# Kernel optimization log

Measured on AMD Instinct MI355X. Metric: run time of the kernel, lower is better.

Reference implementation:

```python
import jax, jax.numpy as jnp
import numpy as np

D_MODEL = 1024

def setup_inputs() -> dict:
    key = jax.random.key(0)
    k1, k2, k3, k4, k5 = jax.random.split(key, 5)
    x = jax.random.normal(k1, (4, 2048, D_MODEL), dtype=jnp.float32)
    # torch nn.Linear weights: [out_features, in_features]
    W_qkv = jax.random.normal(k2, (3 * D_MODEL, D_MODEL), dtype=jnp.float32) * (1.0 / np.sqrt(D_MODEL))
    b_qkv = jax.random.normal(k3, (3 * D_MODEL,), dtype=jnp.float32) * 0.01
    W_proj = jax.random.normal(k4, (D_MODEL, D_MODEL), dtype=jnp.float32) * (1.0 / np.sqrt(D_MODEL))
    b_proj = jax.random.normal(k5, (D_MODEL,), dtype=jnp.float32) * 0.01
    return {"x": x, "W_qkv": W_qkv, "b_qkv": b_qkv, "W_proj": W_proj, "b_proj": b_proj}

def reference(x, W_qkv, b_qkv, W_proj, b_proj):
    # qkv projection: x @ W.T + b  (torch Linear convention)
    qkv = jnp.einsum('bsd,ed->bse', x, W_qkv) + b_qkv  # [B,S,3D]
    q, k, v = jnp.split(qkv, 3, axis=-1)               # each [B,S,D]
    scale = 1.0 / jnp.sqrt(jnp.asarray(q.shape[-1], dtype=q.dtype))
    scores = jnp.einsum('bqd,bkd->bqk', q, k) * scale   # [B,S,S]
    attn = jax.nn.softmax(scores, axis=-1)
    out = jnp.einsum('bqk,bkd->bqd', attn, v)           # [B,S,D]
    return jnp.einsum('bsd,ed->bse', out, W_proj) + b_proj
```

## Files before the change

### kernel.cpp

```cpp
#include <hip/hip_runtime.h>
#include <stdint.h>
#include <stddef.h>


typedef __attribute__((ext_vector_type(8))) short bf16x8;
typedef __attribute__((ext_vector_type(4))) float f32x4;

__device__ __forceinline__ unsigned short f2bf(float f) {
  unsigned u = __float_as_uint(f);
  u += 0x7fffu + ((u >> 16) & 1u);
  return (unsigned short)(u >> 16);
}
__device__ __forceinline__ float bf2f(unsigned short h) {
  return __uint_as_float(((unsigned)h) << 16);
}

typedef const __attribute__((address_space(1))) void* gas_ptr;
typedef __attribute__((address_space(3))) void* las_ptr;

__device__ __forceinline__ void gload_lds16(const void* g, void* l) {
  __builtin_amdgcn_global_load_lds((gas_ptr)(uintptr_t)g,
                                   (las_ptr)(uint32_t)(uintptr_t)l, 16, 0, 0);
}

__device__ __forceinline__ f32x4 mfma16(bf16x8 a, bf16x8 b, f32x4 c) {
  return __builtin_amdgcn_mfma_f32_16x16x32_bf16(a, b, c, 0, 0, 0);
}

__global__ __launch_bounds__(256) void cvt_f32_bf16(
    const float* __restrict__ in, unsigned short* __restrict__ out, int n) {
  int i = (blockIdx.x * blockDim.x + threadIdx.x) * 4;
  int stride = gridDim.x * blockDim.x * 4;
  for (; i < n; i += stride) {
    float4 v = *reinterpret_cast<const float4*>(in + i);
    ushort4 o;
    o.x = f2bf(v.x); o.y = f2bf(v.y); o.z = f2bf(v.z); o.w = f2bf(v.w);
    *reinterpret_cast<ushort4*>(out + i) = o;
  }
}

__device__ __forceinline__ void stage_gf(const unsigned short* __restrict__ P,
                                         int ld, unsigned short* dst, int wid,
                                         int lane) {
#pragma unroll
  for (int c = 0; c < 4; ++c) {
    int s = (c * 4 + wid) * 64 + lane;
    int row = s >> 3, g = s & 7;
    gload_lds16(P + (size_t)row * ld + ((g ^ (row & 7)) * 8),
                dst + (c * 4 + wid) * 512);
  }
}

template <bool OUT_BF16, bool HAS_BIAS, bool EXPOUT, bool RSCALE,
          bool TRANSOUT, bool RSUM>
__global__ __launch_bounds__(256, 2) void gf(
    const unsigned short* __restrict__ A, const unsigned short* __restrict__ B,
    void* __restrict__ Cv, const float* __restrict__ bias,
    const float* __restrict__ rowsc, float* __restrict__ rsum, int rsStride,
    int K, int lda, int ldb, int ldc,
    long long strideA, long long strideB, long long strideC, float alpha) {
  __shared__ unsigned short lds[2][2][128 * 64];

  const int bz = blockIdx.z;
  const int gx = gridDim.x;
  int lin = blockIdx.y * gx + blockIdx.x;
  int bx, by;
  {
    const int nwg = gx * gridDim.y;
    const int q = nwg >> 3;
    lin = (lin & 7) * q + (lin >> 3);
    const int t = lin >> 6, r = lin & 63;
    const int tilesX = gx >> 3;
    bx = (t % tilesX) * 8 + (r & 7);
    by = (t / tilesX) * 8 + (r >> 3);
  }
  const int rowBase = by * 128;
  const int colBase = bx * 128;

  const unsigned short* Ap = A + (size_t)bz * (size_t)strideA + (size_t)rowBase * lda;
  const unsigned short* Bp = B + (size_t)bz * (size_t)strideB + (size_t)colBase * ldb;

  const int tid = threadIdx.x;
  const int wid = tid >> 6;
  const int lane = tid & 63;
  const int wr = wid >> 1;
  const int wc = wid & 1;
  const int fr = lane & 15;
  const int kgi = lane >> 4;

  const int nt = K >> 6;

  f32x4 acc[4][4] = {};

  stage_gf(Ap, lda, &lds[0][0][0], wid, lane);
  stage_gf(Bp, ldb, &lds[0][1][0], wid, lane);
  asm volatile("s_waitcnt vmcnt(0)" ::: "memory");
  __builtin_amdgcn_sched_barrier(0);
  __builtin_amdgcn_s_barrier();

  for (int t = 0; t < nt; ++t) {
    const int cur = t & 1;
    if (t + 1 < nt) {
      stage_gf(Ap + (size_t)(t + 1) * 64, lda, &lds[cur ^ 1][0][0], wid, lane);
      stage_gf(Bp + (size_t)(t + 1) * 64, ldb, &lds[cur ^ 1][1][0], wid, lane);
    }
    const unsigned short* sAc = &lds[cur][0][0];
    const unsigned short* sBc = &lds[cur][1][0];

    bf16x8 af[4][2], bv[4][2];
#pragma unroll
    for (int m = 0; m < 4; ++m) {
      int row = wr * 64 + m * 16 + fr;
      int r7 = row & 7;
      af[m][0] = *(const bf16x8*)&sAc[row * 64 + ((kgi ^ r7) * 8)];
      af[m][1] = *(const bf16x8*)&sAc[row * 64 + (((4 + kgi) ^ r7) * 8)];
    }
#pragma unroll
    for (int n = 0; n < 4; ++n) {
      int row = wc * 64 + n * 16 + fr;
      int r7 = row & 7;
      bv[n][0] = *(const bf16x8*)&sBc[row * 64 + ((kgi ^ r7) * 8)];
      bv[n][1] = *(const bf16x8*)&sBc[row * 64 + (((4 + kgi) ^ r7) * 8)];
    }
    asm volatile("s_waitcnt lgkmcnt(0)" ::: "memory");
    __builtin_amdgcn_sched_barrier(0);
    __builtin_amdgcn_s_setprio(1);
#pragma unroll
    for (int m = 0; m < 4; ++m)
#pragma unroll
      for (int n = 0; n < 4; ++n) {
        acc[m][n] = mfma16(af[m][0], bv[n][0], acc[m][n]);
        acc[m][n] = mfma16(af[m][1], bv[n][1], acc[m][n]);
      }
    __builtin_amdgcn_s_setprio(0);
    __builtin_amdgcn_sched_barrier(0);
    asm volatile("s_waitcnt vmcnt(0)" ::: "memory");
    __builtin_amdgcn_sched_barrier(0);
    __builtin_amdgcn_s_barrier();
  }

  const int rg = (lane >> 4) * 4;
  const float* rsb = RSCALE ? rowsc + (size_t)bz * (size_t)rsStride : nullptr;

  if (TRANSOUT) {
    unsigned short* cl = &lds[0][0][0];
#pragma unroll
    for (int m = 0; m < 4; ++m) {
      int rloc0 = wr * 64 + m * 16 + rg;
#pragma unroll
      for (int n = 0; n < 4; ++n) {
        int cloc = wc * 64 + n * 16 + fr;
        float bvs = HAS_BIAS ? bias[colBase + cloc] : 0.0f;
#pragma unroll
        for (int j = 0; j < 4; ++j) {
          float v = acc[m][n][j] * alpha + bvs;
          cl[cloc * 136 + rloc0 + j] = f2bf(v);
        }
      }
    }
    __syncthreads();
    const int b = rowBase >> 11;
    const int s0 = rowBase & 2047;
    unsigned short* Vt = reinterpret_cast<unsigned short*>(Cv);
#pragma unroll
    for (int i = 0; i < 8; ++i) {
      int slot = i * 256 + tid;
      int d = slot >> 4, sg = slot & 15;
      bf16x8 v = *(const bf16x8*)&cl[d * 136 + sg * 8];
      *(bf16x8*)&Vt[((size_t)(b * 1024 + colBase + d)) * 2048 + s0 + sg * 8] = v;
    }
  } else if (OUT_BF16) {
    unsigned short* cl = &lds[0][0][0];
#pragma unroll
    for (int m = 0; m < 4; ++m) {
      int rloc0 = wr * 64 + m * 16 + rg;
      float rs4[4];
      if (RSCALE) {
#pragma unroll
        for (int j = 0; j < 4; ++j) rs4[j] = rsb[rowBase + rloc0 + j];
      }
#pragma unroll
      for (int n = 0; n < 4; ++n) {
        int cloc = wc * 64 + n * 16 + fr;
        float bvs = 0.0f;
        if (HAS_BIAS) bvs = bias[colBase + cloc];
#pragma unroll
        for (int j = 0; j < 4; ++j) {
          int row = rloc0 + j;
          float v = acc[m][n][j] * alpha;
          if (EXPOUT) v = __expf(v);
          else v += bvs;
          if (RSCALE) v *= rs4[j];
          int gW = cloc >> 3;
          int gS = (gW & 8) | ((gW & 7) ^ (row & 7));
          cl[row * 128 + gS * 8 + (cloc & 7)] = f2bf(v);
        }
      }
    }
    __syncthreads();
    unsigned short* Cb =
        reinterpret_cast<unsigned short*>(Cv) + (size_t)bz * (size_t)strideC;
#pragma unroll
    for (int i = 0; i < 8; ++i) {
      int slot = i * 256 + tid;
      int row = slot >> 4, g = slot & 15;
      int gS = (g & 8) | ((g & 7) ^ (row & 7));
      bf16x8 v = *(const bf16x8*)&cl[row * 128 + gS * 8];
      *(bf16x8*)&Cb[(size_t)(rowBase + row) * ldc + colBase + g * 8] = v;
      if (RSUM) {
        float s8 = 0.0f;
#pragma unroll
        for (int k = 0; k < 8; ++k) s8 += bf2f((unsigned short)v[k]);
        s8 += __shfl_xor(s8, 1);
        s8 += __shfl_xor(s8, 2);
        s8 += __shfl_xor(s8, 4);
        s8 += __shfl_xor(s8, 8);
        if ((lane & 15) == 0)
          rsum[((size_t)bz * 2048 + rowBase + row) * 16 + bx] = s8;
      }
    }
  } else {
    float* clf = reinterpret_cast<float*>(&lds[0][0][0]);
#pragma unroll
    for (int m = 0; m < 4; ++m) {
      int rloc0 = wr * 64 + m * 16 + rg;
      float rs4[4];
      if (RSCALE) {
#pragma unroll
        for (int j = 0; j < 4; ++j) rs4[j] = rsb[rowBase + rloc0 + j];
      }
#pragma unroll
      for (int n = 0; n < 4; ++n) {
        int cloc = wc * 64 + n * 16 + fr;
        float bvs = 0.0f;
        if (HAS_BIAS) bvs = bias[colBase + cloc];
#pragma unroll
        for (int j = 0; j < 4; ++j) {
          int row = rloc0 + j;
          float v = acc[m][n][j] * alpha;
          if (EXPOUT) v = __expf(v);
          else v += bvs;
          if (RSCALE) v *= rs4[j];
          int gW = cloc >> 2;
          int gS = (gW & 24) | ((gW & 7) ^ (row & 7));
          clf[row * 128 + gS * 4 + (cloc & 3)] = v;
        }
      }
    }
    __syncthreads();
    float* Cf = reinterpret_cast<float*>(Cv) + (size_t)bz * (size_t)strideC;
#pragma unroll
    for (int i = 0; i < 16; ++i) {
      int slot = i * 256 + tid;
      int row = slot >> 5, g = slot & 31;
      int gS = (g & 24) | ((g & 7) ^ (row & 7));
      float4 v = *(const float4*)&clf[row * 128 + gS * 4];
      *(float4*)&Cf[(size_t)(rowBase + row) * ldc + colBase + g * 4] = v;
    }
  }
}

__global__ __launch_bounds__(256) void inv_from_partial(
    const float* __restrict__ rs, float* __restrict__ inv) {
  int r = blockIdx.x * 256 + threadIdx.x;
  const float4* p = reinterpret_cast<const float4*>(rs + (size_t)r * 16);
  float4 a = p[0], b = p[1], c = p[2], d = p[3];
  float s = a.x + a.y + a.z + a.w + b.x + b.y + b.z + b.w +
            c.x + c.y + c.z + c.w + d.x + d.y + d.z + d.w;
  inv[r] = 1.0f / s;
}

extern "C" void kernel_launch(void* const* d_in, const int* in_sizes, int n_in,
                              void* d_out, int out_size, void* d_ws, size_t ws_size,
                              hipStream_t stream) {
  const float* x     = (const float*)d_in[0];
  const float* Wqkv  = (const float*)d_in[1];
  const float* bqkv  = (const float*)d_in[2];
  const float* Wproj = (const float*)d_in[3];
  const float* bproj = (const float*)d_in[4];
  float* out = (float*)d_out;

  char* ws = (char*)d_ws;
  unsigned short* qk   = (unsigned short*)(ws + 0);
  unsigned short* xatt = (unsigned short*)(ws + 50331648);
  unsigned short* wq   = (unsigned short*)(ws + 67108864);
  float*          invs = (float*)(ws + 33554432);
  float*          rsp  = (float*)(ws + 33554432 + 65536);
  unsigned short* wp   = (unsigned short*)(ws + 73400320);
  unsigned short* vt   = (unsigned short*)(ws + 75497472);
  unsigned short* sc   = (unsigned short*)(ws + 92274688);

  dim3 blk256(256);

  cvt_f32_bf16<<<2048, blk256, 0, stream>>>(x, xatt, 8192 * 1024);
  cvt_f32_bf16<<<1024, blk256, 0, stream>>>(Wqkv, wq, 3072 * 1024);
  cvt_f32_bf16<<<512, blk256, 0, stream>>>(Wproj, wp, 1024 * 1024);

  gf<true, true, false, false, false, false><<<dim3(16, 64, 1), blk256, 0, stream>>>(
      xatt, wq, qk, bqkv, nullptr, nullptr, 0,
      1024, 1024, 1024, 2048, 0, 0, 0, 1.0f);

  gf<true, true, false, false, true, false><<<dim3(8, 64, 1), blk256, 0, stream>>>(
      xatt, wq + 2048 * 1024, vt, bqkv + 2048, nullptr, nullptr, 0,
      1024, 1024, 1024, 2048, 0, 0, 0, 1.0f);

  gf<true, false, true, false, false, true><<<dim3(16, 16, 4), blk256, 0, stream>>>(
      qk, qk + 1024, sc, nullptr, nullptr, rsp, 0,
      1024, 2048, 2048, 2048,
      2048LL * 2048, 2048LL * 2048, 2048LL * 2048, 0.03125f);

  inv_from_partial<<<32, blk256, 0, stream>>>(rsp, invs);

  gf<true, false, false, true, false, false><<<dim3(8, 16, 4), blk256, 0, stream>>>(
      sc, vt, xatt, nullptr, invs, nullptr, 2048,
      2048, 2048, 2048, 1024,
      2048LL * 2048, 1024LL * 2048, 2048LL * 1024, 1.0f);

  gf<false, true, false, false, false, false><<<dim3(8, 64, 1), blk256, 0, stream>>>(
      xatt, wp, out, bproj, nullptr, nullptr, 0,
      1024, 1024, 1024, 1024, 0, 0, 0, 1.0f);
}
```

Before: 176.9 us.

## Compute softmax row sums via MFMA with ones vector inside PV GEMM

Drops the row-sum reduction from the exp-score GEMM epilogue and the separate inverse kernel. The P·V GEMM now computes each row's sum by running extra MFMAs of the A fragments against a vector of bf16 ones, then scales the output by the reciprocal. This removes one kernel launch, the partial-sum writes and reads, and the shuffle reductions. In exchange it adds 8 MFMAs per k-step to the 32 already there, and each of the 8 column blocks recomputes the same sums redundantly.

```diff
diff --git a/kernel.cpp b/kernel.cpp
--- a/kernel.cpp
+++ b/kernel.cpp
@@ -51,12 +51,10 @@
   }
 }
 
-template <bool OUT_BF16, bool HAS_BIAS, bool EXPOUT, bool RSCALE,
-          bool TRANSOUT, bool RSUM>
+template <bool OUT_BF16, bool HAS_BIAS, bool EXPOUT, bool TRANSOUT, bool RINV>
 __global__ __launch_bounds__(256, 2) void gf(
     const unsigned short* __restrict__ A, const unsigned short* __restrict__ B,
     void* __restrict__ Cv, const float* __restrict__ bias,
-    const float* __restrict__ rowsc, float* __restrict__ rsum, int rsStride,
     int K, int lda, int ldb, int ldc,
     long long strideA, long long strideB, long long strideC, float alpha) {
   __shared__ unsigned short lds[2][2][128 * 64];
@@ -91,6 +89,10 @@
   const int nt = K >> 6;
 
   f32x4 acc[4][4] = {};
+  f32x4 rsacc[4] = {};
+  bf16x8 ones;
+#pragma unroll
+  for (int i = 0; i < 8; ++i) ones[i] = (short)0x3F80;
 
   stage_gf(Ap, lda, &lds[0][0][0], wid, lane);
   stage_gf(Bp, ldb, &lds[0][1][0], wid, lane);
@@ -132,6 +134,13 @@
         acc[m][n] = mfma16(af[m][0], bv[n][0], acc[m][n]);
         acc[m][n] = mfma16(af[m][1], bv[n][1], acc[m][n]);
       }
+    if (RINV) {
+#pragma unroll
+      for (int m = 0; m < 4; ++m) {
+        rsacc[m] = mfma16(af[m][0], ones, rsacc[m]);
+        rsacc[m] = mfma16(af[m][1], ones, rsacc[m]);
+      }
+    }
     __builtin_amdgcn_s_setprio(0);
     __builtin_amdgcn_sched_barrier(0);
     asm volatile("s_waitcnt vmcnt(0)" ::: "memory");
@@ -140,7 +149,6 @@
   }
 
   const int rg = (lane >> 4) * 4;
-  const float* rsb = RSCALE ? rowsc + (size_t)bz * (size_t)rsStride : nullptr;
 
   if (TRANSOUT) {
     unsigned short* cl = &lds[0][0][0];
@@ -175,9 +183,9 @@
     for (int m = 0; m < 4; ++m) {
       int rloc0 = wr * 64 + m * 16 + rg;
       float rs4[4];
-      if (RSCALE) {
-#pragma unroll
-        for (int j = 0; j < 4; ++j) rs4[j] = rsb[rowBase + rloc0 + j];
+      if (RINV) {
+#pragma unroll
+        for (int j = 0; j < 4; ++j) rs4[j] = 1.0f / rsacc[m][j];
       }
 #pragma unroll
       for (int n = 0; n < 4; ++n) {
@@ -190,7 +198,7 @@
           float v = acc[m][n][j] * alpha;
           if (EXPOUT) v = __expf(v);
           else v += bvs;
-          if (RSCALE) v *= rs4[j];
+          if (RINV) v *= rs4[j];
           int gW = cloc >> 3;
           int gS = (gW & 8) | ((gW & 7) ^ (row & 7));
           cl[row * 128 + gS * 8 + (cloc & 7)] = f2bf(v);
@@ -207,28 +215,12 @@
       int gS = (g & 8) | ((g & 7) ^ (row & 7));
       bf16x8 v = *(const bf16x8*)&cl[row * 128 + gS * 8];
       *(bf16x8*)&Cb[(size_t)(rowBase + row) * ldc + colBase + g * 8] = v;
-      if (RSUM) {
-        float s8 = 0.0f;
-#pragma unroll
-        for (int k = 0; k < 8; ++k) s8 += bf2f((unsigned short)v[k]);
-        s8 += __shfl_xor(s8, 1);
-        s8 += __shfl_xor(s8, 2);
-        s8 += __shfl_xor(s8, 4);
-        s8 += __shfl_xor(s8, 8);
-        if ((lane & 15) == 0)
-          rsum[((size_t)bz * 2048 + rowBase + row) * 16 + bx] = s8;
-      }
     }
   } else {
     float* clf = reinterpret_cast<float*>(&lds[0][0][0]);
 #pragma unroll
     for (int m = 0; m < 4; ++m) {
       int rloc0 = wr * 64 + m * 16 + rg;
-      float rs4[4];
-      if (RSCALE) {
-#pragma unroll
-        for (int j = 0; j < 4; ++j) rs4[j] = rsb[rowBase + rloc0 + j];
-      }
 #pragma unroll
       for (int n = 0; n < 4; ++n) {
         int cloc = wc * 64 + n * 16 + fr;
@@ -237,10 +229,7 @@
 #pragma unroll
         for (int j = 0; j < 4; ++j) {
           int row = rloc0 + j;
-          float v = acc[m][n][j] * alpha;
-          if (EXPOUT) v = __expf(v);
-          else v += bvs;
-          if (RSCALE) v *= rs4[j];
+          float v = acc[m][n][j] * alpha + bvs;
           int gW = cloc >> 2;
           int gS = (gW & 24) | ((gW & 7) ^ (row & 7));
           clf[row * 128 + gS * 4 + (cloc & 3)] = v;
@@ -258,16 +247,6 @@
       *(float4*)&Cf[(size_t)(rowBase + row) * ldc + colBase + g * 4] = v;
     }
   }
-}
-
-__global__ __launch_bounds__(256) void inv_from_partial(
-    const float* __restrict__ rs, float* __restrict__ inv) {
-  int r = blockIdx.x * 256 + threadIdx.x;
-  const float4* p = reinterpret_cast<const float4*>(rs + (size_t)r * 16);
-  float4 a = p[0], b = p[1], c = p[2], d = p[3];
-  float s = a.x + a.y + a.z + a.w + b.x + b.y + b.z + b.w +
-            c.x + c.y + c.z + c.w + d.x + d.y + d.z + d.w;
-  inv[r] = 1.0f / s;
 }
 
 extern "C" void kernel_launch(void* const* d_in, const int* in_sizes, int n_in,
@@ -284,8 +263,6 @@
   unsigned short* qk   = (unsigned short*)(ws + 0);
   unsigned short* xatt = (unsigned short*)(ws + 50331648);
   unsigned short* wq   = (unsigned short*)(ws + 67108864);
-  float*          invs = (float*)(ws + 33554432);
-  float*          rsp  = (float*)(ws + 33554432 + 65536);
   unsigned short* wp   = (unsigned short*)(ws + 73400320);
   unsigned short* vt   = (unsigned short*)(ws + 75497472);
   unsigned short* sc   = (unsigned short*)(ws + 92274688);
@@ -296,27 +273,25 @@
   cvt_f32_bf16<<<1024, blk256, 0, stream>>>(Wqkv, wq, 3072 * 1024);
   cvt_f32_bf16<<<512, blk256, 0, stream>>>(Wproj, wp, 1024 * 1024);
 
-  gf<true, true, false, false, false, false><<<dim3(16, 64, 1), blk256, 0, stream>>>(
-      xatt, wq, qk, bqkv, nullptr, nullptr, 0,
+  gf<true, true, false, false, false><<<dim3(16, 64, 1), blk256, 0, stream>>>(
+      xatt, wq, qk, bqkv,
       1024, 1024, 1024, 2048, 0, 0, 0, 1.0f);
 
-  gf<true, true, false, false, true, false><<<dim3(8, 64, 1), blk256, 0, stream>>>(
-      xatt, wq + 2048 * 1024, vt, bqkv + 2048, nullptr, nullptr, 0,
+  gf<true, true, false, true, false><<<dim3(8, 64, 1), blk256, 0, stream>>>(
+      xatt, wq + 2048 * 1024, vt, bqkv + 2048,
       1024, 1024, 1024, 2048, 0, 0, 0, 1.0f);
 
-  gf<true, false, true, false, false, true><<<dim3(16, 16, 4), blk256, 0, stream>>>(
-      qk, qk + 1024, sc, nullptr, nullptr, rsp, 0,
+  gf<true, false, true, false, false><<<dim3(16, 16, 4), blk256, 0, stream>>>(
+      qk, qk + 1024, sc, nullptr,
       1024, 2048, 2048, 2048,
       2048LL * 2048, 2048LL * 2048, 2048LL * 2048, 0.03125f);
 
-  inv_from_partial<<<32, blk256, 0, stream>>>(rsp, invs);
-
-  gf<true, false, false, true, false, false><<<dim3(8, 16, 4), blk256, 0, stream>>>(
-      sc, vt, xatt, nullptr, invs, nullptr, 2048,
+  gf<true, false, false, false, true><<<dim3(8, 16, 4), blk256, 0, stream>>>(
+      sc, vt, xatt, nullptr,
       2048, 2048, 2048, 1024,
       2048LL * 2048, 1024LL * 2048, 2048LL * 1024, 1.0f);
 
-  gf<false, true, false, false, false, false><<<dim3(8, 64, 1), blk256, 0, stream>>>(
-      xatt, wp, out, bproj, nullptr, nullptr, 0,
+  gf<false, true, false, false, false><<<dim3(8, 64, 1), blk256, 0, stream>>>(
+      xatt, wp, out, bproj,
       1024, 1024, 1024, 1024, 0, 0, 0, 1.0f);
 }
```

After: 176.6 us. Within noise of the previous version (-0.2%).
